# Kernel tuning notes

Hardware: AMD Instinct MI355X
Metric: run time of the kernel (lower is better)

The kernel has to match this reference:

```python
import jax, jax.numpy as jnp
import numpy as np

N = 100000   # nodes
F = 64       # features
K = 5        # filter taps
E = 1600000  # edges per sparse power (avg degree 16)


def setup_inputs() -> dict:
    key = jax.random.key(0)
    k1, k2, k3, k4, k5 = jax.random.split(key, 5)
    x = jax.random.normal(k1, (N, F), dtype=jnp.float32)
    h = jax.random.normal(k2, (K,), dtype=jnp.float32)
    vals = jax.random.normal(k3, (K, E), dtype=jnp.float32)
    rows = jax.random.randint(k4, (K, E), 0, N, dtype=jnp.int32)
    cols = jax.random.randint(k5, (K, E), 0, N, dtype=jnp.int32)
    return {"x": x, "h": h, "vals": vals, "rows": rows, "cols": cols}


def reference(x, h, vals, rows, cols):
    # H = sum_k h[k] * S_k  (COO);  out = H @ x
    # Fuse the weighted sum of K sparse matrices directly into one SpMM:
    # scale each power's values by h[k], flatten all K edge lists, and
    # scatter-add the gathered rows of x.
    n = x.shape[0]
    w = (h[:, None] * vals).reshape(-1)          # [K*E]
    r = rows.reshape(-1)                         # [K*E]
    c = cols.reshape(-1)                         # [K*E]
    contrib = x[c] * w[:, None]                  # [K*E, F] gather + scale
    out = jax.ops.segment_sum(contrib, r, num_segments=n)  # [N, F]
    return out
```

## Files before the change

### kernel.cpp

```cpp
#include <hip/hip_runtime.h>
#include <hip/hip_bf16.h>


#define RPB   64
#define SUB   2
#define GWG   128

static __global__ __launch_bounds__(1024) void count_kernel(
    const int* __restrict__ rows, int* __restrict__ cnt,
    int KE, int NSTREAM, int chunk)
{
    extern __shared__ int hist[];
    const int g = blockIdx.x;
    for (int j = threadIdx.x; j < NSTREAM; j += blockDim.x) hist[j] = 0;
    __syncthreads();
    const int lo = g * chunk;
    const int hi = min(lo + chunk, KE);
    for (int e = lo + threadIdx.x; e < hi; e += blockDim.x) {
        const int r = rows[e];
        atomicAdd(&hist[((r >> 6) << 1) | (r & 1)], 1);
    }
    __syncthreads();
    for (int j = threadIdx.x; j < NSTREAM; j += blockDim.x)
        cnt[(size_t)j * GWG + g] = hist[j];
}

static __global__ __launch_bounds__(GWG) void scan1_kernel(
    int* __restrict__ cnt, int* __restrict__ ssBeg)
{
    __shared__ int tmp[GWG];
    const int s = blockIdx.x;
    const int t = threadIdx.x;
    const int v = cnt[(size_t)s * GWG + t];
    tmp[t] = v;
    __syncthreads();
    for (int d = 1; d < GWG; d <<= 1) {
        int u = (t >= d) ? tmp[t - d] : 0;
        __syncthreads();
        tmp[t] += u;
        __syncthreads();
    }
    cnt[(size_t)s * GWG + t] = tmp[t] - v;
    if (t == GWG - 1) ssBeg[s] = tmp[t];
}

static __global__ __launch_bounds__(1024) void scan2_kernel(
    int* __restrict__ a, int n)
{
    __shared__ int sums[1024];
    const int t = threadIdx.x;
    const int chunk = (n + 1023) >> 10;
    const int lo = t * chunk;
    const int hi = min(lo + chunk, n);
    int s = 0;
    for (int i = lo; i < hi; ++i) s += a[i];
    sums[t] = s;
    __syncthreads();
    for (int d = 1; d < 1024; d <<= 1) {
        int v = (t >= d) ? sums[t - d] : 0;
        __syncthreads();
        sums[t] += v;
        __syncthreads();
    }
    int run = (t > 0) ? sums[t - 1] : 0;
    for (int i = lo; i < hi; ++i) {
        const int cv = a[i];
        a[i] = run;
        run += cv;
    }
    if (t == 1023) a[n] = sums[1023];
}

static __global__ __launch_bounds__(1024) void scan3_kernel(
    int* __restrict__ cnt, const int* __restrict__ ssBeg, int total)
{
    const int i = blockIdx.x * blockDim.x + threadIdx.x;
    if (i < total) cnt[i] += ssBeg[i >> 7];
}

static __global__ __launch_bounds__(1024) void scatter_kernel(
    const int*   __restrict__ rows,
    const int*   __restrict__ cols,
    const float* __restrict__ vals,
    const float* __restrict__ h,
    const int*   __restrict__ cnt,
    int2*        __restrict__ payload,
    int KE, int E, int K, int NSTREAM, int chunk)
{
    extern __shared__ int lcur[];
    const int g = blockIdx.x;
    for (int j = threadIdx.x; j < NSTREAM; j += blockDim.x)
        lcur[j] = cnt[(size_t)j * GWG + g];
    __syncthreads();
    const int lo = g * chunk;
    const int hi = min(lo + chunk, KE);
    if (lo >= hi) return;
    const int k0 = lo / E;
    const int k1 = min((hi - 1) / E, K - 1);
    for (int k = k0; k <= k1; ++k) {
        const float hk = h[k];
        const int s0 = max(lo, k * E);
        const int s1 = min(hi, (k + 1) * E);
        for (int e = s0 + threadIdx.x; e < s1; e += blockDim.x) {
            const int r = rows[e];
            const int st = ((r >> 6) << 1) | (r & 1);
            const int pos = atomicAdd(&lcur[st], 1);
            payload[pos] = make_int2(((r & 63) << 17) | cols[e],
                                     __float_as_int(hk * vals[e]));
        }
    }
}

static __global__ __launch_bounds__(256) void convert_kernel(
    const float* __restrict__ x, ushort* __restrict__ xh, int n4)
{
    const int i = blockIdx.x * blockDim.x + threadIdx.x;
    if (i >= n4) return;
    const float4 v = ((const float4*)x)[i];
    ushort4 o;
    o.x = __bfloat16_as_ushort(__float2bfloat16(v.x));
    o.y = __bfloat16_as_ushort(__float2bfloat16(v.y));
    o.z = __bfloat16_as_ushort(__float2bfloat16(v.z));
    o.w = __bfloat16_as_ushort(__float2bfloat16(v.w));
    ((ushort4*)xh)[i] = o;
}

static __global__ __launch_bounds__(128) void spmv_bf16_kernel(
    const int*    __restrict__ ssBeg,
    const int2*   __restrict__ payload,
    const ushort* __restrict__ xh,
    float*        __restrict__ out,
    int N)
{
    __shared__ float acc[RPB * 64];
    const int b = blockIdx.x;
    for (int i = threadIdx.x; i < RPB * 64; i += 128) acc[i] = 0.f;
    __syncthreads();

    const int lane = threadIdx.x & 63;
    const int wv   = threadIdx.x >> 6;
    const int s    = b * SUB + wv;
    int e        = ssBeg[s];
    const int be = ssBeg[s + 1];

    while (e + 16 <= be) {
        int2 pa[8], pb[8];
        float xa[8], xb[8];
        #pragma unroll
        for (int j = 0; j < 8; ++j) pa[j] = payload[e + j];
        #pragma unroll
        for (int j = 0; j < 8; ++j) pb[j] = payload[e + 8 + j];
        #pragma unroll
        for (int j = 0; j < 8; ++j)
            xa[j] = __bfloat162float(__ushort_as_bfloat16(
                        xh[(size_t)(pa[j].x & 0x1FFFF) * 64 + lane]));
        #pragma unroll
        for (int j = 0; j < 8; ++j)
            xb[j] = __bfloat162float(__ushort_as_bfloat16(
                        xh[(size_t)(pb[j].x & 0x1FFFF) * 64 + lane]));
        #pragma unroll
        for (int j = 0; j < 8; ++j)
            acc[(pa[j].x >> 17) * 64 + lane] += __int_as_float(pa[j].y) * xa[j];
        #pragma unroll
        for (int j = 0; j < 8; ++j)
            acc[(pb[j].x >> 17) * 64 + lane] += __int_as_float(pb[j].y) * xb[j];
        e += 16;
    }
    for (; e < be; ++e) {
        const int2 p = payload[e];
        const float xv = __bfloat162float(__ushort_as_bfloat16(
                             xh[(size_t)(p.x & 0x1FFFF) * 64 + lane]));
        acc[(p.x >> 17) * 64 + lane] += __int_as_float(p.y) * xv;
    }
    __syncthreads();

    const int base = b * RPB;
    const int nrow = min(RPB, N - base);
    for (int i = threadIdx.x; i < nrow * 64; i += 128)
        out[(size_t)base * 64 + i] = acc[i];
}

static __global__ __launch_bounds__(128) void spmv_f32_kernel(
    const int*  __restrict__ ssBeg,
    const int2* __restrict__ payload,
    const float* __restrict__ x,
    float*       __restrict__ out,
    int N)
{
    __shared__ float acc[RPB * 64];
    const int b = blockIdx.x;
    for (int i = threadIdx.x; i < RPB * 64; i += 128) acc[i] = 0.f;
    __syncthreads();

    const int lane = threadIdx.x & 63;
    const int wv   = threadIdx.x >> 6;
    const int s    = b * SUB + wv;
    int e        = ssBeg[s];
    const int be = ssBeg[s + 1];

    while (e + 16 <= be) {
        int2 pa[8], pb[8];
        float xa[8], xb[8];
        #pragma unroll
        for (int j = 0; j < 8; ++j) pa[j] = payload[e + j];
        #pragma unroll
        for (int j = 0; j < 8; ++j) pb[j] = payload[e + 8 + j];
        #pragma unroll
        for (int j = 0; j < 8; ++j)
            xa[j] = x[(size_t)(pa[j].x & 0x1FFFF) * 64 + lane];
        #pragma unroll
        for (int j = 0; j < 8; ++j)
            xb[j] = x[(size_t)(pb[j].x & 0x1FFFF) * 64 + lane];
        #pragma unroll
        for (int j = 0; j < 8; ++j)
            acc[(pa[j].x >> 17) * 64 + lane] += __int_as_float(pa[j].y) * xa[j];
        #pragma unroll
        for (int j = 0; j < 8; ++j)
            acc[(pb[j].x >> 17) * 64 + lane] += __int_as_float(pb[j].y) * xb[j];
        e += 16;
    }
    for (; e < be; ++e) {
        const int2 p = payload[e];
        acc[(p.x >> 17) * 64 + lane] +=
            __int_as_float(p.y) * x[(size_t)(p.x & 0x1FFFF) * 64 + lane];
    }
    __syncthreads();

    const int base = b * RPB;
    const int nrow = min(RPB, N - base);
    for (int i = threadIdx.x; i < nrow * 64; i += 128)
        out[(size_t)base * 64 + i] = acc[i];
}

static __global__ __launch_bounds__(256) void gtconv_scatter(
    const float* __restrict__ x, const float* __restrict__ h,
    const float* __restrict__ vals, const int* __restrict__ rows,
    const int* __restrict__ cols, float* __restrict__ out, int KE, int E)
{
    const int lane = threadIdx.x & 63;
    int wave = (blockIdx.x * blockDim.x + threadIdx.x) >> 6;
    const int nwaves = (gridDim.x * blockDim.x) >> 6;
    for (int e = wave; e < KE; e += nwaves) {
        float w = h[e / E] * vals[e];
        float xv = x[(size_t)cols[e] * 64 + lane];
        unsafeAtomicAdd(&out[(size_t)rows[e] * 64 + lane], xv * w);
    }
}

extern "C" void kernel_launch(void* const* d_in, const int* in_sizes, int n_in,
                              void* d_out, int out_size, void* d_ws, size_t ws_size,
                              hipStream_t stream) {
    const float* x    = (const float*)d_in[0];
    const float* h    = (const float*)d_in[1];
    const float* vals = (const float*)d_in[2];
    const int*   rows = (const int*)d_in[3];
    const int*   cols = (const int*)d_in[4];
    float* out = (float*)d_out;

    const int K  = in_sizes[1];
    const int KE = in_sizes[2];
    const int E  = KE / K;
    const int F  = 64;
    const int N  = in_sizes[0] / F;
    const int NB      = (N + RPB - 1) / RPB;
    const int NSTREAM = NB * SUB;

    const size_t lds_need = (size_t)NSTREAM * 4;
    const size_t cnt_off  = 0;
    const size_t cnt_sz   = (size_t)NSTREAM * GWG * 4;
    const size_t ss_off   = cnt_off + cnt_sz;
    const size_t ss_sz    = (size_t)(NSTREAM + 1) * 4;
    const size_t pl_off   = (ss_off + ss_sz + 15) & ~(size_t)15;
    const size_t base_need = pl_off + (size_t)KE * 8;
    const size_t xh_off   = (base_need + 15) & ~(size_t)15;
    const size_t full_need = xh_off + (size_t)N * F * 2;

    if (ws_size < base_need || lds_need > 64 * 1024) {
        hipMemsetAsync(out, 0, (size_t)out_size * sizeof(float), stream);
        gtconv_scatter<<<8192, 256, 0, stream>>>(x, h, vals, rows, cols, out, KE, E);
        return;
    }

    char* ws = (char*)d_ws;
    int*    cnt     = (int*)(ws + cnt_off);
    int*    ssBeg   = (int*)(ws + ss_off);
    int2*   payload = (int2*)(ws + pl_off);
    ushort* xh      = (ushort*)(ws + xh_off);
    const bool use_bf16 = (ws_size >= full_need);

    const int chunk = (KE + GWG - 1) / GWG;

    if (use_bf16) {
        const int n4 = (N * F) / 4;
        convert_kernel<<<(n4 + 255) / 256, 256, 0, stream>>>(x, xh, n4);
    }
    count_kernel<<<GWG, 1024, lds_need, stream>>>(rows, cnt, KE, NSTREAM, chunk);
    scan1_kernel<<<NSTREAM, GWG, 0, stream>>>(cnt, ssBeg);
    scan2_kernel<<<1, 1024, 0, stream>>>(ssBeg, NSTREAM);
    const int total = NSTREAM * GWG;
    scan3_kernel<<<(total + 1023) / 1024, 1024, 0, stream>>>(cnt, ssBeg, total);
    scatter_kernel<<<GWG, 1024, lds_need, stream>>>(rows, cols, vals, h, cnt,
                                                    payload, KE, E, K, NSTREAM, chunk);
    if (use_bf16)
        spmv_bf16_kernel<<<NB, 128, 0, stream>>>(ssBeg, payload, xh, out, N);
    else
        spmv_f32_kernel<<<NB, 128, 0, stream>>>(ssBeg, payload, x, out, N);
}
```

Measured before the change: 391.2 us.

## Replace per-workgroup offset scan with global atomic cursors in scatter

Count now accumulates per-stream totals into a global array with atomics, and a single scan kernel produces the stream offsets plus padded global cursors, one per 64-byte slot. This removes two of the three scan kernels and the large per-workgroup count matrix. The scatter now runs with many more smaller workgroups that claim payload slots through global atomics instead of LDS cursors. This cuts launch overhead and raises scatter parallelism, at the cost of heavy global atomic contention (about 8M atomics on about 3.1K addresses) and a nondeterministic edge order within each stream.

```diff
diff --git a/kernel.cpp b/kernel.cpp
--- a/kernel.cpp
+++ b/kernel.cpp
@@ -2,12 +2,13 @@
 #include <hip/hip_bf16.h>
 
 
-#define RPB   64
-#define SUB   2
-#define GWG   128
+#define RPB    64
+#define SUB    2
+#define GWG_C  256
+#define GWG_S  1024
 
 static __global__ __launch_bounds__(1024) void count_kernel(
-    const int* __restrict__ rows, int* __restrict__ cnt,
+    const int* __restrict__ rows, int* __restrict__ cntTot,
     int KE, int NSTREAM, int chunk)
 {
     extern __shared__ int hist[];
@@ -21,31 +22,15 @@
         atomicAdd(&hist[((r >> 6) << 1) | (r & 1)], 1);
     }
     __syncthreads();
-    for (int j = threadIdx.x; j < NSTREAM; j += blockDim.x)
-        cnt[(size_t)j * GWG + g] = hist[j];
-}
-
-static __global__ __launch_bounds__(GWG) void scan1_kernel(
-    int* __restrict__ cnt, int* __restrict__ ssBeg)
-{
-    __shared__ int tmp[GWG];
-    const int s = blockIdx.x;
-    const int t = threadIdx.x;
-    const int v = cnt[(size_t)s * GWG + t];
-    tmp[t] = v;
-    __syncthreads();
-    for (int d = 1; d < GWG; d <<= 1) {
-        int u = (t >= d) ? tmp[t - d] : 0;
-        __syncthreads();
-        tmp[t] += u;
-        __syncthreads();
-    }
-    cnt[(size_t)s * GWG + t] = tmp[t] - v;
-    if (t == GWG - 1) ssBeg[s] = tmp[t];
-}
-
-static __global__ __launch_bounds__(1024) void scan2_kernel(
-    int* __restrict__ a, int n)
+    for (int j = threadIdx.x; j < NSTREAM; j += blockDim.x) {
+        const int v = hist[j];
+        if (v) atomicAdd(&cntTot[j], v);
+    }
+}
+
+static __global__ __launch_bounds__(1024) void scan_kernel(
+    const int* __restrict__ cntTot, int* __restrict__ ssBeg,
+    int* __restrict__ cursor, int n)
 {
     __shared__ int sums[1024];
     const int t = threadIdx.x;
@@ -53,7 +38,7 @@
     const int lo = t * chunk;
     const int hi = min(lo + chunk, n);
     int s = 0;
-    for (int i = lo; i < hi; ++i) s += a[i];
+    for (int i = lo; i < hi; ++i) s += cntTot[i];
     sums[t] = s;
     __syncthreads();
     for (int d = 1; d < 1024; d <<= 1) {
@@ -64,34 +49,24 @@
     }
     int run = (t > 0) ? sums[t - 1] : 0;
     for (int i = lo; i < hi; ++i) {
-        const int cv = a[i];
-        a[i] = run;
+        const int cv = cntTot[i];
+        ssBeg[i] = run;
+        cursor[(size_t)i * 16] = run;
         run += cv;
     }
-    if (t == 1023) a[n] = sums[1023];
-}
-
-static __global__ __launch_bounds__(1024) void scan3_kernel(
-    int* __restrict__ cnt, const int* __restrict__ ssBeg, int total)
-{
-    const int i = blockIdx.x * blockDim.x + threadIdx.x;
-    if (i < total) cnt[i] += ssBeg[i >> 7];
-}
-
-static __global__ __launch_bounds__(1024) void scatter_kernel(
+    if (t == 1023) ssBeg[n] = sums[1023];
+}
+
+static __global__ __launch_bounds__(256) void scatter_kernel(
     const int*   __restrict__ rows,
     const int*   __restrict__ cols,
     const float* __restrict__ vals,
     const float* __restrict__ h,
-    const int*   __restrict__ cnt,
+    int*         __restrict__ cursor,
     int2*        __restrict__ payload,
-    int KE, int E, int K, int NSTREAM, int chunk)
-{
-    extern __shared__ int lcur[];
+    int KE, int E, int K, int chunk)
+{
     const int g = blockIdx.x;
-    for (int j = threadIdx.x; j < NSTREAM; j += blockDim.x)
-        lcur[j] = cnt[(size_t)j * GWG + g];
-    __syncthreads();
     const int lo = g * chunk;
     const int hi = min(lo + chunk, KE);
     if (lo >= hi) return;
@@ -104,7 +79,7 @@
         for (int e = s0 + threadIdx.x; e < s1; e += blockDim.x) {
             const int r = rows[e];
             const int st = ((r >> 6) << 1) | (r & 1);
-            const int pos = atomicAdd(&lcur[st], 1);
+            const int pos = atomicAdd(&cursor[(size_t)st * 16], 1);
             payload[pos] = make_int2(((r & 63) << 17) | cols[e],
                                      __float_as_int(hk * vals[e]));
         }
@@ -265,14 +240,13 @@
     const int NB      = (N + RPB - 1) / RPB;
     const int NSTREAM = NB * SUB;
 
-    const size_t lds_need = (size_t)NSTREAM * 4;
-    const size_t cnt_off  = 0;
-    const size_t cnt_sz   = (size_t)NSTREAM * GWG * 4;
-    const size_t ss_off   = cnt_off + cnt_sz;
-    const size_t ss_sz    = (size_t)(NSTREAM + 1) * 4;
-    const size_t pl_off   = (ss_off + ss_sz + 15) & ~(size_t)15;
+    const size_t lds_need  = (size_t)NSTREAM * 4;
+    const size_t ct_off    = 0;
+    const size_t ss_off    = ct_off + (size_t)NSTREAM * 4;
+    const size_t cur_off   = (ss_off + (size_t)(NSTREAM + 1) * 4 + 63) & ~(size_t)63;
+    const size_t pl_off    = (cur_off + (size_t)NSTREAM * 64 + 15) & ~(size_t)15;
     const size_t base_need = pl_off + (size_t)KE * 8;
-    const size_t xh_off   = (base_need + 15) & ~(size_t)15;
+    const size_t xh_off    = (base_need + 15) & ~(size_t)15;
     const size_t full_need = xh_off + (size_t)N * F * 2;
 
     if (ws_size < base_need || lds_need > 64 * 1024) {
@@ -282,25 +256,25 @@
     }
 
     char* ws = (char*)d_ws;
-    int*    cnt     = (int*)(ws + cnt_off);
+    int*    cntTot  = (int*)(ws + ct_off);
     int*    ssBeg   = (int*)(ws + ss_off);
+    int*    cursor  = (int*)(ws + cur_off);
     int2*   payload = (int2*)(ws + pl_off);
     ushort* xh      = (ushort*)(ws + xh_off);
     const bool use_bf16 = (ws_size >= full_need);
 
-    const int chunk = (KE + GWG - 1) / GWG;
-
+    hipMemsetAsync(cntTot, 0, (size_t)NSTREAM * 4, stream);
     if (use_bf16) {
         const int n4 = (N * F) / 4;
         convert_kernel<<<(n4 + 255) / 256, 256, 0, stream>>>(x, xh, n4);
     }
-    count_kernel<<<GWG, 1024, lds_need, stream>>>(rows, cnt, KE, NSTREAM, chunk);
-    scan1_kernel<<<NSTREAM, GWG, 0, stream>>>(cnt, ssBeg);
-    scan2_kernel<<<1, 1024, 0, stream>>>(ssBeg, NSTREAM);
-    const int total = NSTREAM * GWG;
-    scan3_kernel<<<(total + 1023) / 1024, 1024, 0, stream>>>(cnt, ssBeg, total);
-    scatter_kernel<<<GWG, 1024, lds_need, stream>>>(rows, cols, vals, h, cnt,
-                                                    payload, KE, E, K, NSTREAM, chunk);
+
+    const int chunk_c = (KE + GWG_C - 1) / GWG_C;
+    count_kernel<<<GWG_C, 1024, lds_need, stream>>>(rows, cntTot, KE, NSTREAM, chunk_c);
+    scan_kernel<<<1, 1024, 0, stream>>>(cntTot, ssBeg, cursor, NSTREAM);
+    const int chunk_s = (KE + GWG_S - 1) / GWG_S;
+    scatter_kernel<<<GWG_S, 256, 0, stream>>>(rows, cols, vals, h, cursor,
+                                              payload, KE, E, K, chunk_s);
     if (use_bf16)
         spmv_bf16_kernel<<<NB, 128, 0, stream>>>(ssBeg, payload, xh, out, N);
     else
```

Result: slower. 811.7 us (+107.5%).
